# Performance work log

Measured on AMD Instinct MI355X. Metric: run time of the kernel, lower is better.

## Reference

```python
import jax, jax.numpy as jnp
import numpy as np

B, N = 32, 512


def _stick_breaking(b, x_mask):
    """Row-major stick-breaking recurrence, O(N^2) sequential steps.

    Equivalent to the TF while_loop: for step in range(N*N), m=step//N, n=step%N:
      fut      = max(0, x_mask[:,m,n+1:] - sum_{m'<m} x[:,m',n+1:])  (col partial sums)
      mfm      = sum_j fut_j
      row_sum  = sum_{n'<n} x[:,m,n']
      col_sum  = sum_{m'<m} x[:,m',n]
      lower    = mask[m,n]*max(0, 1 - row_sum - mfm)
      upper    = mask[m,n]*min(1 - row_sum, 1 - col_sum)
      x[m,n]   = lower + b[m,n]*(upper - lower)
    Key insight: during row m the column partial sums are constant, so the
    future-mass terms for every n can be precomputed as an exclusive reverse
    cumsum; only the within-row dependency (row_sum) needs a scan.
    """
    Bb, Nn, _ = b.shape
    dt = b.dtype

    def row_step(col_sums, inputs):
        b_row, mask_row = inputs                      # [B, N] each
        fut = jnp.maximum(0.0, mask_row - col_sums)   # [B, N]
        # mfm[:, n] = sum_{j > n} fut[:, j]  (exclusive reverse cumsum)
        mfm = jnp.flip(jnp.cumsum(jnp.flip(fut, -1), axis=-1), -1) - fut

        def col_step(row_sum, inp):
            b_mn, m_mn, mfm_n, cs_n = inp             # [B] each
            lower = m_mn * jnp.maximum(0.0, 1.0 - row_sum - mfm_n)
            upper = m_mn * jnp.minimum(1.0 - row_sum, 1.0 - cs_n)
            p = lower + b_mn * (upper - lower)
            return row_sum + p, p

        _, row = jax.lax.scan(
            col_step,
            jnp.zeros((Bb,), dt),
            (b_row.T, mask_row.T, mfm.T, col_sums.T),
        )
        row = row.T                                   # [B, N]
        return col_sums + row, row

    _, rows = jax.lax.scan(
        row_step,
        jnp.zeros((Bb, Nn), dt),
        (jnp.swapaxes(b, 0, 1), jnp.swapaxes(x_mask, 0, 1)),
    )
    return jnp.swapaxes(rows, 0, 1)                   # [B, N, N]


def setup_inputs() -> dict:
    key = jax.random.key(0)
    k1, _ = jax.random.split(key)
    x = jax.random.normal(k1, (B, N, N), dtype=jnp.float32)
    x_mask = jnp.ones((B, N, N), dtype=jnp.float32)
    return {"x": x, "x_mask": x_mask}


def reference(x, x_mask):
    # layer.call applies sigmoid to the logits before stick-breaking
    return _stick_breaking(jax.nn.sigmoid(x), x_mask)
```

## Files before the change

### kernel.cpp

```cpp
#include <hip/hip_runtime.h>

#define NBATCH 32
#define NDIM 512
#define NFAST 448
#define NQUAD 112
#define NWAVE 8


__device__ __forceinline__ void prefix_prep(float& p, float rx, float rm,
                                            float& c2n, float& oc2n) {
  float t0, t1, t2;
  asm("v_mul_f32 %1, 0xbfb8aa3b, %6\n\t"
      "s_nop 0\n\t"
      "v_add_f32_dpp %0, %0, %0 row_shr:1 row_mask:0xf bank_mask:0xf\n\t"
      "v_exp_f32 %1, %1\n\t"
      "s_nop 0\n\t"
      "v_add_f32_dpp %0, %0, %0 row_shr:2 row_mask:0xf bank_mask:0xf\n\t"
      "v_add_f32 %2, 1.0, %1\n\t"
      "s_nop 0\n\t"
      "v_add_f32_dpp %0, %0, %0 row_shr:4 row_mask:0xf bank_mask:0xf\n\t"
      "v_rcp_f32 %3, %2\n\t"
      "s_nop 0\n\t"
      "v_add_f32_dpp %0, %0, %0 row_shr:8 row_mask:0xf bank_mask:0xf\n\t"
      "v_mul_f32 %4, %7, %3\n\t"
      "s_nop 0\n\t"
      "v_add_f32_dpp %0, %0, %0 row_bcast:15 row_mask:0xa bank_mask:0xf\n\t"
      "v_sub_f32 %5, 1.0, %4\n\t"
      "s_nop 0\n\t"
      "v_add_f32_dpp %0, %0, %0 row_bcast:31 row_mask:0xc bank_mask:0xf"
      : "+v"(p), "=&v"(t0), "=&v"(t1), "=&v"(t2), "=&v"(c2n), "=&v"(oc2n)
      : "v"(rx), "v"(rm));
}

__device__ __forceinline__ void prefix_inc2(float& a, float& b) {
  asm("s_nop 1\n\t"
      "v_add_f32_dpp %0, %0, %0 row_shr:1 row_mask:0xf bank_mask:0xf\n\t"
      "v_add_f32_dpp %1, %1, %1 row_shr:1 row_mask:0xf bank_mask:0xf\n\t"
      "s_nop 0\n\t"
      "v_add_f32_dpp %0, %0, %0 row_shr:2 row_mask:0xf bank_mask:0xf\n\t"
      "v_add_f32_dpp %1, %1, %1 row_shr:2 row_mask:0xf bank_mask:0xf\n\t"
      "s_nop 0\n\t"
      "v_add_f32_dpp %0, %0, %0 row_shr:4 row_mask:0xf bank_mask:0xf\n\t"
      "v_add_f32_dpp %1, %1, %1 row_shr:4 row_mask:0xf bank_mask:0xf\n\t"
      "s_nop 0\n\t"
      "v_add_f32_dpp %0, %0, %0 row_shr:8 row_mask:0xf bank_mask:0xf\n\t"
      "v_add_f32_dpp %1, %1, %1 row_shr:8 row_mask:0xf bank_mask:0xf\n\t"
      "s_nop 0\n\t"
      "v_add_f32_dpp %0, %0, %0 row_bcast:15 row_mask:0xa bank_mask:0xf\n\t"
      "v_add_f32_dpp %1, %1, %1 row_bcast:15 row_mask:0xa bank_mask:0xf\n\t"
      "s_nop 0\n\t"
      "v_add_f32_dpp %0, %0, %0 row_bcast:31 row_mask:0xc bank_mask:0xf\n\t"
      "v_add_f32_dpp %1, %1, %1 row_bcast:31 row_mask:0xc bank_mask:0xf\n\t"
      "s_nop 1"
      : "+v"(a), "+v"(b));
}

__device__ __forceinline__ void aff_scan(float& A, float& B) {
  asm("s_nop 1\n\t"
      "v_fmac_f32_dpp %1, %1, %0 row_shr:1 row_mask:0xf bank_mask:0xf\n\t"
      "v_mul_f32_dpp  %0, %0, %0 row_shr:1 row_mask:0xf bank_mask:0xf\n\t"
      "s_nop 0\n\t"
      "v_fmac_f32_dpp %1, %1, %0 row_shr:2 row_mask:0xf bank_mask:0xf\n\t"
      "v_mul_f32_dpp  %0, %0, %0 row_shr:2 row_mask:0xf bank_mask:0xf\n\t"
      "s_nop 0\n\t"
      "v_fmac_f32_dpp %1, %1, %0 row_shr:4 row_mask:0xf bank_mask:0xf\n\t"
      "v_mul_f32_dpp  %0, %0, %0 row_shr:4 row_mask:0xf bank_mask:0xf\n\t"
      "s_nop 0\n\t"
      "v_fmac_f32_dpp %1, %1, %0 row_shr:8 row_mask:0xf bank_mask:0xf\n\t"
      "v_mul_f32_dpp  %0, %0, %0 row_shr:8 row_mask:0xf bank_mask:0xf\n\t"
      "s_nop 0\n\t"
      "v_fmac_f32_dpp %1, %1, %0 row_bcast:15 row_mask:0xa bank_mask:0xf\n\t"
      "v_mul_f32_dpp  %0, %0, %0 row_bcast:15 row_mask:0xa bank_mask:0xf\n\t"
      "s_nop 0\n\t"
      "v_fmac_f32_dpp %1, %1, %0 row_bcast:31 row_mask:0xc bank_mask:0xf\n\t"
      "v_mul_f32_dpp  %0, %0, %0 row_bcast:31 row_mask:0xc bank_mask:0xf\n\t"
      "s_nop 1"
      : "+v"(A), "+v"(B));
}

__device__ __forceinline__ float wave_shr1(float x, float fill) {
  return __int_as_float(__builtin_amdgcn_update_dpp(
      __float_as_int(fill), __float_as_int(x), 0x138 , 0xf, 0xf,
      false));
}

__device__ __forceinline__ void wg_barrier() {
  asm volatile("s_waitcnt lgkmcnt(0)" ::: "memory");
  __builtin_amdgcn_s_barrier();
  asm volatile("" ::: "memory");
}

__global__ __launch_bounds__(512, 2)
void sb_kernel(const float* __restrict__ x, const float* __restrict__ xm,
               float* __restrict__ out) {
  const int tid = (int)threadIdx.x;
  const int lane = tid & 63;
  const int w = __builtin_amdgcn_readfirstlane(tid >> 6);
  const size_t base =
      (size_t)blockIdx.x * NDIM * NDIM + (size_t)(w * 64 + lane);
  const float* xb = x + base;
  const float* mb = xm + base;
  float* ob = out + base;

  __shared__ float4 recs[NFAST];
  __shared__ alignas(16) float ex_sa[NWAVE];
  __shared__ alignas(16) float ex_S[NWAVE];
  __shared__ alignas(16) float ex_A[NWAVE];
  __shared__ alignas(16) float ex_B[NWAVE];

  float w8, t8;
  float c2_0, oc2_0, c2_1, oc2_1, c2_2, oc2_2, c2_3, oc2_3;
  float c1, c2, oc2;
  float fu = 0.0f, S = 0.0f;

  float X0 = xb[0], X1 = xb[NDIM], X2 = xb[2 * NDIM], X3 = xb[3 * NDIM];
  float M0 = mb[0], M1 = mb[NDIM], M2 = mb[2 * NDIM], M3 = mb[3 * NDIM];
  float q1x0 = xb[4 * NDIM], q1x1 = xb[5 * NDIM], q1x2 = xb[6 * NDIM],
        q1x3 = xb[7 * NDIM];
  float q1m0 = mb[4 * NDIM], q1m1 = mb[5 * NDIM], q1m2 = mb[6 * NDIM],
        q1m3 = mb[7 * NDIM];
  float Ax0 = q1x0, Ax1 = q1x1, Ax2 = q1x2, Ax3 = q1x3;
  float Am0 = q1m0, Am1 = q1m1, Am2 = q1m2, Am3 = q1m3;
  float Bx0 = q1x0, Bx1 = q1x1, Bx2 = q1x2, Bx3 = q1x3;
  float Bm0 = q1m0, Bm1 = q1m1, Bm2 = q1m2, Bm3 = q1m3;

  {
    float s0 = __builtin_amdgcn_rcpf(1.0f + __expf(-X0));
    float s1 = __builtin_amdgcn_rcpf(1.0f + __expf(-X1));
    float s2 = __builtin_amdgcn_rcpf(1.0f + __expf(-X2));
    float s3 = __builtin_amdgcn_rcpf(1.0f + __expf(-X3));
    c2_0 = M0 * s0;
    oc2_0 = 1.0f - c2_0;
    c2_1 = M1 * s1;
    oc2_1 = 1.0f - c2_1;
    c2_2 = M2 * s2;
    oc2_2 = 1.0f - c2_2;
    c2_3 = M3 * s3;
    oc2_3 = 1.0f - c2_3;
    w8 = 1.0f;
    t8 = c2_0;
  }

  const float* px = xb + (long)(8 - 4 * w) * NDIM;
  const float* pm = mb + (long)(8 - 4 * w) * NDIM;
  float* po = ob - (long)(4 * w) * NDIM;

  auto row_fast = [&](int m, const float4& r, float c2r, float oc2r,
                      float rx, float rm, float& c2n, float& oc2n,
                      float* pO) {
    float PA = t8;
    prefix_prep(PA, rx, rm, c2n, oc2n);
    float uin = fmaxf(1.0f - (r.z + (PA - t8)), 0.0f);
    bool pW = w8 < uin;
    float A = pW ? 1.0f : oc2r;
    float Bv = pW ? (-t8) : 0.0f;
    aff_scan(A, Bv);
    float Aex = wave_shr1(A, 1.0f);
    float Bex = wave_shr1(Bv, 0.0f);
    if (w < NWAVE - 1 && lane == 63)
      recs[m] = make_float4(A * r.x, fmaf(A, r.y, Bv), r.z + PA, 0.0f);
    float E = r.x + r.y;
    float e = fminf(fmaxf(fmaf(Aex, E, Bex), 0.0f), 1.0f);
    float p = c2r * fminf(e, w8);
    w8 -= p;
    *pO = p;
  };

  auto quad_step = [&](int t, int k, float& WX0, float& WX1, float& WX2,
                       float& WX3, float& WM0, float& WM1, float& WM2,
                       float& WM3, const float& RX0, const float& RX1,
                       const float& RX2, const float& RX3, const float& RM0,
                       const float& RM1, const float& RM2, const float& RM3) {
    const int q = t - w;
    if ((unsigned)q < (unsigned)NQUAD) {
      const int m = 4 * q;
      float4 r0 = make_float4(1.0f, 0.0f, 0.0f, 0.0f);
      float4 r1 = r0, r2 = r0, r3 = r0;
      if (w > 0) {
        r0 = recs[m];
        r1 = recs[m + 1];
        r2 = recs[m + 2];
        r3 = recs[m + 3];
      }
      const float* pxk = px + (size_t)(4 * k) * NDIM;
      const float* pmk = pm + (size_t)(4 * k) * NDIM;
      WX0 = pxk[0];
      WX1 = pxk[NDIM];
      WX2 = pxk[2 * NDIM];
      WX3 = pxk[3 * NDIM];
      WM0 = pmk[0];
      WM1 = pmk[NDIM];
      WM2 = pmk[2 * NDIM];
      WM3 = pmk[3 * NDIM];

      float c2n0, oc2n0, c2n1, oc2n1, c2n2, oc2n2, c2n3, oc2n3;
      float* pok = po + (size_t)(4 * k) * NDIM;
      row_fast(m + 0, r0, c2_0, oc2_0, RX0, RM0, c2n0, oc2n0, pok);
      t8 = c2_1 * w8;
      row_fast(m + 1, r1, c2_1, oc2_1, RX1, RM1, c2n1, oc2n1, pok + NDIM);
      t8 = c2_2 * w8;
      row_fast(m + 2, r2, c2_2, oc2_2, RX2, RM2, c2n2, oc2n2,
               pok + 2 * NDIM);
      t8 = c2_3 * w8;
      row_fast(m + 3, r3, c2_3, oc2_3, RX3, RM3, c2n3, oc2n3,
               pok + 3 * NDIM);
      t8 = c2n0 * w8;
      c2_0 = c2n0;
      oc2_0 = oc2n0;
      c2_1 = c2n1;
      oc2_1 = oc2n1;
      c2_2 = c2n2;
      oc2_2 = oc2n2;
      c2_3 = c2n3;
      oc2_3 = oc2n3;
    }
    wg_barrier();
  };

#pragma unroll 1
  for (int t = 0; t < NQUAD + NWAVE; t += 2) {
    quad_step(t + 0, 0, Ax0, Ax1, Ax2, Ax3, Am0, Am1, Am2, Am3, Bx0, Bx1, Bx2,
              Bx3, Bm0, Bm1, Bm2, Bm3);
    quad_step(t + 1, 1, Bx0, Bx1, Bx2, Bx3, Bm0, Bm1, Bm2, Bm3, Ax0, Ax1, Ax2,
              Ax3, Am0, Am1, Am2, Am3);
    px += 8 * NDIM;
    pm += 8 * NDIM;
    po += 8 * NDIM;
  }

  float fx0, fm0, fx1, fm1, fx2, fm2, fx3, fm3;
  {
    float m448 = mb[(size_t)448 * NDIM];
    fx1 = xb[(size_t)449 * NDIM];
    fm1 = mb[(size_t)449 * NDIM];
    fx2 = xb[(size_t)450 * NDIM];
    fm2 = mb[(size_t)450 * NDIM];
    fx3 = xb[(size_t)451 * NDIM];
    fm3 = mb[(size_t)451 * NDIM];
    fx0 = fx1;
    fm0 = fm1;
    c2 = c2_0;
    oc2 = oc2_0;
    c1 = m448 - c2;
    float om = 1.0f - m448;
    fu = fmaxf(w8 - om, 0.0f);
    S = fu;
  }

  auto row_full = [&](int m, float& WX, float& WM, const float& RX,
                      const float& RM) {
    const size_t nro = (size_t)((m + 4) & (NDIM - 1)) * NDIM;
    WX = xb[nro];
    WM = mb[nro];

    float PS = S, PA = t8;
    prefix_inc2(PS, PA);

    if (lane == 63) {
      ex_sa[w] = PA;
      ex_S[w] = PS;
    }
    wg_barrier();

    float4 sl = *(const float4*)&ex_sa[0];
    float4 sh = *(const float4*)&ex_sa[4];
    float4 Sl = *(const float4*)&ex_S[0];
    float4 Sh = *(const float4*)&ex_S[4];
    float off_sa = 0.0f, off_S = 0.0f;
    if (w > 0) { off_sa += sl.x; off_S += Sl.x; }
    if (w > 1) { off_sa += sl.y; off_S += Sl.y; }
    if (w > 2) { off_sa += sl.z; off_S += Sl.z; }
    if (w > 3) { off_sa += sl.w; off_S += Sl.w; }
    if (w > 4) { off_sa += sh.x; off_S += Sh.x; }
    if (w > 5) { off_sa += sh.y; off_S += Sh.y; }
    if (w > 6) { off_sa += sh.z; off_S += Sh.z; }
    float Tg =
        ((Sl.x + Sl.y) + (Sl.z + Sl.w)) + ((Sh.x + Sh.y) + (Sh.z + Sh.w));

    float uin = fmaxf(1.0f - (off_sa + (PA - t8)), 0.0f);
    float R_ = (Tg - off_S) - PS;
    float nc1m = -c1 * R_;

    bool pW = w8 < uin;
    float aP = pW ? 1.0f : oc2;
    float bP = pW ? (-t8) : 0.0f;
    bool pL = (uin - R_) > 0.0f;
    if (pL) {
      aP -= c1;
      bP -= nc1m;
    }

    float A = aP, Bv = bP;
    aff_scan(A, Bv);
    float Aex = wave_shr1(A, 1.0f);
    float Bex = wave_shr1(Bv, 0.0f);

    if (lane == 63) {
      ex_A[w] = A;
      ex_B[w] = Bv;
    }
    wg_barrier();

    float4 Al = *(const float4*)&ex_A[0];
    float4 Ah = *(const float4*)&ex_A[4];
    float4 Bl = *(const float4*)&ex_B[0];
    float4 Bh = *(const float4*)&ex_B[4];
    float E = 1.0f;
    if (w > 0) E = fmaf(Al.x, E, Bl.x);
    if (w > 1) E = fmaf(Al.y, E, Bl.y);
    if (w > 2) E = fmaf(Al.z, E, Bl.z);
    if (w > 3) E = fmaf(Al.w, E, Bl.w);
    if (w > 4) E = fmaf(Ah.x, E, Bh.x);
    if (w > 5) E = fmaf(Ah.y, E, Bh.y);
    if (w > 6) E = fmaf(Ah.z, E, Bh.z);
    float e = fminf(fmaxf(fmaf(Aex, E, Bex), 0.0f), 1.0f);

    float sg = __builtin_amdgcn_rcpf(1.0f + __expf(-RX));
    float c2n = RM * sg;
    float oc2n = 1.0f - c2n;
    float c1n = RM - c2n;
    float omn = 1.0f - RM;

    float U = fminf(e, w8);
    float g = fmaxf(fmaf(c1, e, nc1m), 0.0f);
    float p = fmaf(c2, U, g);
    w8 -= p;
    ob[(size_t)m * NDIM] = p;

    t8 = c2n * w8;
    fu = fmaxf(w8 - omn, 0.0f);
    S = fu;
    c2 = c2n;
    oc2 = oc2n;
    c1 = c1n;
  };

#pragma unroll 1
  for (int m = NFAST; m < NDIM; m += 4) {
    row_full(m + 0, fx0, fm0, fx1, fm1);
    row_full(m + 1, fx1, fm1, fx2, fm2);
    row_full(m + 2, fx2, fm2, fx3, fm3);
    row_full(m + 3, fx3, fm3, fx0, fm0);
  }
}

extern "C" void kernel_launch(void* const* d_in, const int* in_sizes, int n_in,
                              void* d_out, int out_size, void* d_ws,
                              size_t ws_size, hipStream_t stream) {
  const float* x = (const float*)d_in[0];
  const float* xmask = (const float*)d_in[1];
  float* out = (float*)d_out;
  (void)in_sizes;
  (void)n_in;
  (void)out_size;
  (void)d_ws;
  (void)ws_size;
  hipLaunchKernelGGL(sb_kernel, dim3(NBATCH), dim3(512), 0, stream, x, xmask,
                     out);
}
```

Baseline: 236.4 us.

## Process eight rows per barrier step and fuse exclusive shift into affine scan

The wavefront-pipelined fast phase now handles eight rows per workgroup barrier instead of four, halving the number of barriers and pipeline steps across the 448 fast rows. The affine prefix scan is fused with the computation of E and the record prefix, and the exclusive shift is applied once to the combined value instead of shifting A and B separately. In exchange, register pressure rises from the 8-wide register arrays and double-buffered prefetch, and the pipeline fill and drain latency per wave doubles.

```diff
diff --git a/kernel.cpp b/kernel.cpp
--- a/kernel.cpp
+++ b/kernel.cpp
@@ -3,7 +3,7 @@
 #define NBATCH 32
 #define NDIM 512
 #define NFAST 448
-#define NQUAD 112
+#define NOCT 56
 #define NWAVE 8
 
 
@@ -76,6 +76,31 @@
       "v_mul_f32_dpp  %0, %0, %0 row_bcast:31 row_mask:0xc bank_mask:0xf\n\t"
       "s_nop 1"
       : "+v"(A), "+v"(B));
+}
+
+__device__ __forceinline__ void aff_scan_f(float& A, float& B, float& E,
+                                           float& P, float rx, float ry,
+                                           float rz, float PA) {
+  asm("s_nop 1\n\t"
+      "v_fmac_f32_dpp %1, %1, %0 row_shr:1 row_mask:0xf bank_mask:0xf\n\t"
+      "v_mul_f32_dpp  %0, %0, %0 row_shr:1 row_mask:0xf bank_mask:0xf\n\t"
+      "v_add_f32 %2, %4, %5\n\t"
+      "v_fmac_f32_dpp %1, %1, %0 row_shr:2 row_mask:0xf bank_mask:0xf\n\t"
+      "v_mul_f32_dpp  %0, %0, %0 row_shr:2 row_mask:0xf bank_mask:0xf\n\t"
+      "v_add_f32 %3, %6, %7\n\t"
+      "v_fmac_f32_dpp %1, %1, %0 row_shr:4 row_mask:0xf bank_mask:0xf\n\t"
+      "v_mul_f32_dpp  %0, %0, %0 row_shr:4 row_mask:0xf bank_mask:0xf\n\t"
+      "s_nop 0\n\t"
+      "v_fmac_f32_dpp %1, %1, %0 row_shr:8 row_mask:0xf bank_mask:0xf\n\t"
+      "v_mul_f32_dpp  %0, %0, %0 row_shr:8 row_mask:0xf bank_mask:0xf\n\t"
+      "s_nop 0\n\t"
+      "v_fmac_f32_dpp %1, %1, %0 row_bcast:15 row_mask:0xa bank_mask:0xf\n\t"
+      "v_mul_f32_dpp  %0, %0, %0 row_bcast:15 row_mask:0xa bank_mask:0xf\n\t"
+      "s_nop 0\n\t"
+      "v_fmac_f32_dpp %1, %1, %0 row_bcast:31 row_mask:0xc bank_mask:0xf\n\t"
+      "v_mul_f32_dpp  %0, %0, %0 row_bcast:31 row_mask:0xc bank_mask:0xf"
+      : "+v"(A), "+v"(B), "=&v"(E), "=&v"(P)
+      : "v"(rx), "v"(ry), "v"(rz), "v"(PA));
 }
 
 __device__ __forceinline__ float wave_shr1(float x, float fill) {
@@ -109,41 +134,35 @@
   __shared__ alignas(16) float ex_B[NWAVE];
 
   float w8, t8;
-  float c2_0, oc2_0, c2_1, oc2_1, c2_2, oc2_2, c2_3, oc2_3;
+  float c2c[8], oc2c[8];
   float c1, c2, oc2;
   float fu = 0.0f, S = 0.0f;
 
-  float X0 = xb[0], X1 = xb[NDIM], X2 = xb[2 * NDIM], X3 = xb[3 * NDIM];
-  float M0 = mb[0], M1 = mb[NDIM], M2 = mb[2 * NDIM], M3 = mb[3 * NDIM];
-  float q1x0 = xb[4 * NDIM], q1x1 = xb[5 * NDIM], q1x2 = xb[6 * NDIM],
-        q1x3 = xb[7 * NDIM];
-  float q1m0 = mb[4 * NDIM], q1m1 = mb[5 * NDIM], q1m2 = mb[6 * NDIM],
-        q1m3 = mb[7 * NDIM];
-  float Ax0 = q1x0, Ax1 = q1x1, Ax2 = q1x2, Ax3 = q1x3;
-  float Am0 = q1m0, Am1 = q1m1, Am2 = q1m2, Am3 = q1m3;
-  float Bx0 = q1x0, Bx1 = q1x1, Bx2 = q1x2, Bx3 = q1x3;
-  float Bm0 = q1m0, Bm1 = q1m1, Bm2 = q1m2, Bm3 = q1m3;
-
+  float Ax[8], Am[8], Bx[8], Bm[8];
   {
-    float s0 = __builtin_amdgcn_rcpf(1.0f + __expf(-X0));
-    float s1 = __builtin_amdgcn_rcpf(1.0f + __expf(-X1));
-    float s2 = __builtin_amdgcn_rcpf(1.0f + __expf(-X2));
-    float s3 = __builtin_amdgcn_rcpf(1.0f + __expf(-X3));
-    c2_0 = M0 * s0;
-    oc2_0 = 1.0f - c2_0;
-    c2_1 = M1 * s1;
-    oc2_1 = 1.0f - c2_1;
-    c2_2 = M2 * s2;
-    oc2_2 = 1.0f - c2_2;
-    c2_3 = M3 * s3;
-    oc2_3 = 1.0f - c2_3;
+    float Xr[8], Mr[8];
+#pragma unroll
+    for (int i = 0; i < 8; ++i) {
+      Xr[i] = xb[(size_t)i * NDIM];
+      Mr[i] = mb[(size_t)i * NDIM];
+      float xv = xb[(size_t)(8 + i) * NDIM];
+      float mv = mb[(size_t)(8 + i) * NDIM];
+      Ax[i] = Bx[i] = xv;
+      Am[i] = Bm[i] = mv;
+    }
+#pragma unroll
+    for (int i = 0; i < 8; ++i) {
+      float sg = __builtin_amdgcn_rcpf(1.0f + __expf(-Xr[i]));
+      c2c[i] = Mr[i] * sg;
+      oc2c[i] = 1.0f - c2c[i];
+    }
     w8 = 1.0f;
-    t8 = c2_0;
+    t8 = c2c[0];
   }
 
-  const float* px = xb + (long)(8 - 4 * w) * NDIM;
-  const float* pm = mb + (long)(8 - 4 * w) * NDIM;
-  float* po = ob - (long)(4 * w) * NDIM;
+  const float* px = xb + (long)(16 - 8 * w) * NDIM;
+  const float* pm = mb + (long)(16 - 8 * w) * NDIM;
+  float* po = ob - (long)(8 * w) * NDIM;
 
   auto row_fast = [&](int m, const float4& r, float c2r, float oc2r,
                       float rx, float rm, float& c2n, float& oc2n,
@@ -154,78 +173,61 @@
     bool pW = w8 < uin;
     float A = pW ? 1.0f : oc2r;
     float Bv = pW ? (-t8) : 0.0f;
-    aff_scan(A, Bv);
-    float Aex = wave_shr1(A, 1.0f);
-    float Bex = wave_shr1(Bv, 0.0f);
+    float E, PArec;
+    aff_scan_f(A, Bv, E, PArec, r.x, r.y, r.z, PA);
     if (w < NWAVE - 1 && lane == 63)
-      recs[m] = make_float4(A * r.x, fmaf(A, r.y, Bv), r.z + PA, 0.0f);
-    float E = r.x + r.y;
-    float e = fminf(fmaxf(fmaf(Aex, E, Bex), 0.0f), 1.0f);
-    float p = c2r * fminf(e, w8);
+      recs[m] = make_float4(A * r.x, fmaf(A, r.y, Bv), PArec, 0.0f);
+    float eI = fmaf(A, E, Bv);
+    float e = wave_shr1(eI, E);
+    float U = fminf(fmaxf(e, 0.0f), w8);
+    float p = c2r * U;
     w8 -= p;
     *pO = p;
   };
 
-  auto quad_step = [&](int t, int k, float& WX0, float& WX1, float& WX2,
-                       float& WX3, float& WM0, float& WM1, float& WM2,
-                       float& WM3, const float& RX0, const float& RX1,
-                       const float& RX2, const float& RX3, const float& RM0,
-                       const float& RM1, const float& RM2, const float& RM3) {
+  auto oct_step = [&](int t, int k, float (&WX)[8], float (&WM)[8],
+                      const float (&RX)[8], const float (&RM)[8]) {
     const int q = t - w;
-    if ((unsigned)q < (unsigned)NQUAD) {
-      const int m = 4 * q;
-      float4 r0 = make_float4(1.0f, 0.0f, 0.0f, 0.0f);
-      float4 r1 = r0, r2 = r0, r3 = r0;
+    if ((unsigned)q < (unsigned)NOCT) {
+      const int m = 8 * q;
+      float4 r[8];
+#pragma unroll
+      for (int i = 0; i < 8; ++i) r[i] = make_float4(1.0f, 0.0f, 0.0f, 0.0f);
       if (w > 0) {
-        r0 = recs[m];
-        r1 = recs[m + 1];
-        r2 = recs[m + 2];
-        r3 = recs[m + 3];
+#pragma unroll
+        for (int i = 0; i < 8; ++i) r[i] = recs[m + i];
       }
-      const float* pxk = px + (size_t)(4 * k) * NDIM;
-      const float* pmk = pm + (size_t)(4 * k) * NDIM;
-      WX0 = pxk[0];
-      WX1 = pxk[NDIM];
-      WX2 = pxk[2 * NDIM];
-      WX3 = pxk[3 * NDIM];
-      WM0 = pmk[0];
-      WM1 = pmk[NDIM];
-      WM2 = pmk[2 * NDIM];
-      WM3 = pmk[3 * NDIM];
-
-      float c2n0, oc2n0, c2n1, oc2n1, c2n2, oc2n2, c2n3, oc2n3;
-      float* pok = po + (size_t)(4 * k) * NDIM;
-      row_fast(m + 0, r0, c2_0, oc2_0, RX0, RM0, c2n0, oc2n0, pok);
-      t8 = c2_1 * w8;
-      row_fast(m + 1, r1, c2_1, oc2_1, RX1, RM1, c2n1, oc2n1, pok + NDIM);
-      t8 = c2_2 * w8;
-      row_fast(m + 2, r2, c2_2, oc2_2, RX2, RM2, c2n2, oc2n2,
-               pok + 2 * NDIM);
-      t8 = c2_3 * w8;
-      row_fast(m + 3, r3, c2_3, oc2_3, RX3, RM3, c2n3, oc2n3,
-               pok + 3 * NDIM);
-      t8 = c2n0 * w8;
-      c2_0 = c2n0;
-      oc2_0 = oc2n0;
-      c2_1 = c2n1;
-      oc2_1 = oc2n1;
-      c2_2 = c2n2;
-      oc2_2 = oc2n2;
-      c2_3 = c2n3;
-      oc2_3 = oc2n3;
+      const float* pxk = px + (size_t)(8 * k) * NDIM;
+      const float* pmk = pm + (size_t)(8 * k) * NDIM;
+#pragma unroll
+      for (int i = 0; i < 8; ++i) {
+        WX[i] = pxk[(size_t)i * NDIM];
+        WM[i] = pmk[(size_t)i * NDIM];
+      }
+      float c2n[8], oc2n[8];
+      float* pok = po + (size_t)(8 * k) * NDIM;
+#pragma unroll
+      for (int i = 0; i < 8; ++i) {
+        row_fast(m + i, r[i], c2c[i], oc2c[i], RX[i], RM[i], c2n[i], oc2n[i],
+                 pok + (size_t)i * NDIM);
+        t8 = (i < 7 ? c2c[i + 1] : c2n[0]) * w8;
+      }
+#pragma unroll
+      for (int i = 0; i < 8; ++i) {
+        c2c[i] = c2n[i];
+        oc2c[i] = oc2n[i];
+      }
     }
     wg_barrier();
   };
 
 #pragma unroll 1
-  for (int t = 0; t < NQUAD + NWAVE; t += 2) {
-    quad_step(t + 0, 0, Ax0, Ax1, Ax2, Ax3, Am0, Am1, Am2, Am3, Bx0, Bx1, Bx2,
-              Bx3, Bm0, Bm1, Bm2, Bm3);
-    quad_step(t + 1, 1, Bx0, Bx1, Bx2, Bx3, Bm0, Bm1, Bm2, Bm3, Ax0, Ax1, Ax2,
-              Ax3, Am0, Am1, Am2, Am3);
-    px += 8 * NDIM;
-    pm += 8 * NDIM;
-    po += 8 * NDIM;
+  for (int t = 0; t < NOCT + NWAVE; t += 2) {
+    oct_step(t + 0, 0, Ax, Am, Bx, Bm);
+    oct_step(t + 1, 1, Bx, Bm, Ax, Am);
+    px += 16 * NDIM;
+    pm += 16 * NDIM;
+    po += 16 * NDIM;
   }
 
   float fx0, fm0, fx1, fm1, fx2, fm2, fx3, fm3;
@@ -239,8 +241,8 @@
     fm3 = mb[(size_t)451 * NDIM];
     fx0 = fx1;
     fm0 = fm1;
-    c2 = c2_0;
-    oc2 = oc2_0;
+    c2 = c2c[0];
+    oc2 = oc2c[0];
     c1 = m448 - c2;
     float om = 1.0f - m448;
     fu = fmaxf(w8 - om, 0.0f);
```

Measured after the change: 235.6 us. No clear change (-0.3%).
